# Kernel tuning notes

Measured on AMD Instinct MI355X. Metric: run time of the kernel, lower is better.

Reference implementation:

```python
import jax, jax.numpy as jnp
import numpy as np
from itertools import permutations

BLOCK = 64  # GroupLinear block_size


def _dist_bucket_table():
    # replicates self.distance: log2-style bucketing of token distances [0,1024)
    t = np.zeros(1024, dtype=np.int32)
    for i, th in enumerate([2, 4, 8, 16, 32, 64, 128, 256, 512]):
        t[th:] = i + 1
    return jnp.asarray(t)


def setup_inputs() -> dict:
    key = jax.random.key(0)
    ks = jax.random.split(key, 12)
    B, S, H, NH = 4, 512, 768, 12
    E, TAG, TE, TD, R = 24, 7, 20, 20, 97
    DIN = 2 * H + TE + TD
    hidden_state = jax.random.normal(ks[0], (B, S, H), jnp.float32)
    attention = jax.random.uniform(ks[1], (B, NH, S, S), jnp.float32)
    attention_mask = jnp.ones((B, S), jnp.float32)
    head = jnp.sort(jax.random.randint(ks[2], (B, E), 0, S), axis=-1)
    tail = jnp.sort(jax.random.randint(ks[3], (B, E), 0, S), axis=-1)
    entity_type = jax.random.randint(ks[4], (B, E), 0, TAG)
    type_table = jax.random.normal(ks[5], (TAG, TE), jnp.float32) * 0.02
    dis_table = jax.random.normal(ks[6], (20, TD), jnp.float32) * 0.02
    Wh = jax.random.normal(ks[7], (DIN, H), jnp.float32) * (1.0 / np.sqrt(DIN))
    bh = jnp.zeros((H,), jnp.float32)
    Wt = jax.random.normal(ks[8], (DIN, H), jnp.float32) * (1.0 / np.sqrt(DIN))
    bt = jnp.zeros((H,), jnp.float32)
    # GroupLinear weight reshaped to [n_blocks, BLOCK, BLOCK, R]
    clsW = jax.random.normal(ks[9], (H // BLOCK, BLOCK, BLOCK, R), jnp.float32) * (1.0 / np.sqrt(H * BLOCK))
    clsb = jnp.zeros((R,), jnp.float32)
    return dict(hidden_state=hidden_state, attention=attention,
                attention_mask=attention_mask, head=head, tail=tail,
                entity_type=entity_type, type_table=type_table,
                dis_table=dis_table, Wh=Wh, bh=bh, Wt=Wt, bt=bt,
                clsW=clsW, clsb=clsb)


def reference(hidden_state, attention, attention_mask, head, tail, entity_type,
              type_table, dis_table, Wh, bh, Wt, bt, clsW, clsb):
    E = head.shape[1]
    hts = jnp.asarray(list(permutations(range(E), 2)), dtype=jnp.int32)  # [P,2]
    i0, i1 = hts[:, 0], hts[:, 1]
    dtab = _dist_bucket_table()
    att = attention.sum(axis=1)  # [B,S,S] sum over heads

    def per_sample(h, a, m, hd, tl, et):
        # h:[S,H] a:[S,S] m:[S] hd,tl,et:[E]
        ent_feat = (h[hd] + h[tl]) * 0.5          # [E,H]
        ent_att = (a[hd] + a[tl]) * 0.5           # [E,S]
        ent_tf = type_table[et]                   # [E,TE]
        head_f, tail_f = ent_feat[i0], ent_feat[i1]      # [P,H]
        ht_att = ent_att[i0] * ent_att[i1] * m[None, :]  # [P,S]
        head_ty, tail_ty = ent_tf[i0], ent_tf[i1]        # [P,TE]
        d = dtab[jnp.abs(tl[i0] - hd[i1])]               # [P]
        ht_dist = dis_table[d]                           # [P,TD]
        ht_att = ht_att / (ht_att.sum(-1, keepdims=True) + 1e-20)
        ht_info = ht_att @ h                             # [P,H]
        all_h = jnp.concatenate([head_f, ht_info, head_ty, ht_dist], axis=-1)
        all_t = jnp.concatenate([tail_f, ht_info, tail_ty, ht_dist], axis=-1)
        return all_h, all_t

    all_h, all_t = jax.vmap(per_sample)(hidden_state, att, attention_mask,
                                        head, tail, entity_type)
    all_h = all_h.reshape(-1, all_h.shape[-1])  # [B*P, DIN]
    all_t = all_t.reshape(-1, all_t.shape[-1])
    h1 = jnp.tanh(all_h @ Wh + bh)              # [L,H]
    t1 = jnp.tanh(all_t @ Wt + bt)
    L, H = h1.shape
    nb = H // BLOCK
    x1 = h1.reshape(L, nb, BLOCK)
    x2 = t1.reshape(L, nb, BLOCK)
    # GroupLinear: per-block outer product then linear, fused as einsum
    logits = jnp.einsum('lnb,lnc,nbcr->lr', x1, x2, clsW) + clsb  # [L,R]
    return logits
```

## Files before the change

### kernel.cpp

```cpp
#include <hip/hip_runtime.h>
#include <hip/hip_bf16.h>
#include <math.h>

#define B_ 4
#define S_ 512
#define H_ 768
#define NH_ 12
#define E_ 24
#define TE_ 20
#define TD_ 20
#define R_ 97
#define DIN_ 1576
#define KPAD_ 1600
#define KS_MLP 50
#define MF_MLP 140
#define KS_HTI 16
#define P_ 552
#define L_ 2208
#define NB_ 12
#define NF_ 7

typedef __bf16 bf16x8 __attribute__((ext_vector_type(8)));
typedef float f32x4 __attribute__((ext_vector_type(4)));

__device__ __forceinline__ unsigned short f2bf(float f) {
  union { float f; unsigned u; } c; c.f = f;
  unsigned r = c.u + 0x7FFF + ((c.u >> 16) & 1);
  return (unsigned short)(r >> 16);
}
__device__ __forceinline__ float bf2f(unsigned short b) {
  union { unsigned u; float f; } c; c.u = ((unsigned)b) << 16;
  return c.f;
}
__device__ __forceinline__ unsigned pk2(float a, float b) {
  return (unsigned)f2bf(a) | ((unsigned)f2bf(b) << 16);
}
__device__ __forceinline__ void gload_lds16(const uint4* g, uint4* l) {
  __builtin_amdgcn_global_load_lds(
      (const __attribute__((address_space(1))) unsigned*)(const void*)g,
      (__attribute__((address_space(3))) unsigned*)(void*)l, 16, 0, 0);
}

__global__ void ent_prep(const float* __restrict__ attn, const float* __restrict__ hs,
                         const int* __restrict__ head, const int* __restrict__ tail,
                         float* __restrict__ ent_att, float* __restrict__ ent_feat) {
  int be = blockIdx.x;
  int b = be / E_;
  int hd = head[be], tl = tail[be];
  int tid = threadIdx.x;
  const float* abase = attn + (size_t)b * NH_ * S_ * S_;
  for (int s = tid; s < S_; s += 256) {
    float acc = 0.f;
#pragma unroll
    for (int nh = 0; nh < NH_; ++nh) {
      const float* ap = abase + (size_t)nh * S_ * S_;
      acc += ap[(size_t)hd * S_ + s] + ap[(size_t)tl * S_ + s];
    }
    ent_att[(size_t)be * S_ + s] = 0.5f * acc;
  }
  const float* hb = hs + (size_t)b * S_ * H_;
  for (int k = tid; k < H_; k += 256) {
    ent_feat[(size_t)be * H_ + k] = 0.5f * (hb[(size_t)hd * H_ + k] + hb[(size_t)tl * H_ + k]);
  }
}

__global__ void pair_att(const float* __restrict__ ent_att, const float* __restrict__ mask,
                         const int* __restrict__ head, const int* __restrict__ tail,
                         const int* __restrict__ etype,
                         float* __restrict__ ht_att, int* __restrict__ meta) {
  int l = blockIdx.x;
  int b = l / P_, p = l % P_;
  int i0 = p / (E_ - 1), rem = p % (E_ - 1);
  int i1 = rem + (rem >= i0 ? 1 : 0);
  int tid = threadIdx.x;
  if (tid == 0) {
    meta[0 * L_ + l] = b * E_ + i0;
    meta[1 * L_ + l] = b * E_ + i1;
    meta[2 * L_ + l] = etype[b * E_ + i0];
    meta[3 * L_ + l] = etype[b * E_ + i1];
    int d = abs(tail[b * E_ + i0] - head[b * E_ + i1]);
    int bk = (d >= 2) + (d >= 4) + (d >= 8) + (d >= 16) + (d >= 32) +
             (d >= 64) + (d >= 128) + (d >= 256) + (d >= 512);
    meta[4 * L_ + l] = bk;
  }
  const float* a0 = ent_att + (size_t)(b * E_ + i0) * S_;
  const float* a1 = ent_att + (size_t)(b * E_ + i1) * S_;
  const float* m = mask + (size_t)b * S_;
  float v0 = a0[tid] * a1[tid] * m[tid];
  float v1 = a0[tid + 256] * a1[tid + 256] * m[tid + 256];
  float loc = v0 + v1;
  for (int o = 32; o > 0; o >>= 1) loc += __shfl_down(loc, o, 64);
  __shared__ float red[4];
  if ((tid & 63) == 0) red[tid >> 6] = loc;
  __syncthreads();
  float tot = red[0] + red[1] + red[2] + red[3];
  float inv = 1.f / (tot + 1e-20f);
  ht_att[(size_t)l * S_ + tid] = v0 * inv;
  ht_att[(size_t)l * S_ + tid + 256] = v1 * inv;
}

__global__ void pack_hs(const float* __restrict__ hs, uint4* __restrict__ hsP) {
  int u = blockIdx.x * 256 + threadIdx.x;
  if (u >= B_ * KS_HTI * 48 * 64) return;
  int lane = u & 63;
  int t = u >> 6;
  int nt16 = t % 48;
  int t2 = t / 48;
  int ks = t2 % KS_HTI;
  int b = t2 / KS_HTI;
  int n = nt16 * 16 + (lane & 15);
  int k0 = ks * 32 + ((lane >> 4) << 3);
  const float* src = hs + (size_t)b * S_ * H_;
  unsigned w[4];
#pragma unroll
  for (int q = 0; q < 4; ++q) {
    int k = k0 + 2 * q;
    w[q] = pk2(src[(size_t)k * H_ + n], src[(size_t)(k + 1) * H_ + n]);
  }
  uint4 o; o.x = w[0]; o.y = w[1]; o.z = w[2]; o.w = w[3];
  hsP[u] = o;
}

__global__ void pack_Wmlp(const float* __restrict__ Wh, const float* __restrict__ Wt,
                          uint4* __restrict__ WpH, uint4* __restrict__ WpT) {
  int u = blockIdx.x * 256 + threadIdx.x;
  if (u >= KS_MLP * 48 * 64) return;
  const float* W = blockIdx.y ? Wt : Wh;
  uint4* Wp = blockIdx.y ? WpT : WpH;
  int lane = u & 63;
  int t = u >> 6;
  int nt16 = t % 48;
  int ks = t / 48;
  int n = nt16 * 16 + (lane & 15);
  int k0 = ks * 32 + ((lane >> 4) << 3);
  unsigned w[4];
#pragma unroll
  for (int q = 0; q < 4; ++q) {
    int k = k0 + 2 * q;
    float v0 = (k < DIN_) ? W[(size_t)k * H_ + n] : 0.f;
    float v1 = (k + 1 < DIN_) ? W[(size_t)(k + 1) * H_ + n] : 0.f;
    w[q] = pk2(v0, v1);
  }
  uint4 o; o.x = w[0]; o.y = w[1]; o.z = w[2]; o.w = w[3];
  Wp[u] = o;
}

__global__ void pack_allx(const float* __restrict__ ent_feat, const float* __restrict__ ht_info,
                          const float* __restrict__ ttab, const float* __restrict__ dtab,
                          const int* __restrict__ meta,
                          uint4* __restrict__ axH, uint4* __restrict__ axT) {
  int idx = blockIdx.x * 256 + threadIdx.x;
  int lane = idx & 63;
  int unit = idx >> 6;
  int half = unit / (MF_MLP * KS_MLP);
  int rem = unit % (MF_MLP * KS_MLP);
  int mf = rem / KS_MLP, ks = rem % KS_MLP;
  int row = mf * 16 + (lane & 15);
  int k = ks * 32 + ((lane >> 4) << 3);
  uint4 d; d.x = d.y = d.z = d.w = 0;
  if (row < L_) {
    int frow = meta[half * L_ + row];
    int trow = meta[(2 + half) * L_ + row];
    int db = meta[4 * L_ + row];
    if (k < 768) {
      const float* p = ent_feat + (size_t)frow * H_ + k;
      float4 v0 = *(const float4*)p, v1 = *(const float4*)(p + 4);
      d.x = pk2(v0.x, v0.y); d.y = pk2(v0.z, v0.w);
      d.z = pk2(v1.x, v1.y); d.w = pk2(v1.z, v1.w);
    } else if (k < 1536) {
      const float* p = ht_info + (size_t)row * H_ + (k - 768);
      float4 v0 = *(const float4*)p, v1 = *(const float4*)(p + 4);
      d.x = pk2(v0.x, v0.y); d.y = pk2(v0.z, v0.w);
      d.z = pk2(v1.x, v1.y); d.w = pk2(v1.z, v1.w);
    } else {
      float v[8];
#pragma unroll
      for (int j = 0; j < 8; ++j) {
        int e = k + j;
        v[j] = (e < 1556) ? ttab[trow * TE_ + (e - 1536)]
             : (e < 1576) ? dtab[db * TD_ + (e - 1556)] : 0.f;
      }
      d.x = pk2(v[0], v[1]); d.y = pk2(v[2], v[3]);
      d.z = pk2(v[4], v[5]); d.w = pk2(v[6], v[7]);
    }
  }
  (half ? axT : axH)[(size_t)rem * 64 + lane] = d;
}

__global__ __launch_bounds__(256) void htinfo_mfma(
    const float* __restrict__ htatt, const uint4* __restrict__ hsP,
    float* __restrict__ htinfo) {
  int b = blockIdx.z;
  int m0 = blockIdx.x * 64;
  int nt0 = blockIdx.y * 4;
  int tid = threadIdx.x;
  int wave = tid >> 6, lane = tid & 63;
  int wm = wave & 1, wn = wave >> 1;
  __shared__ __align__(16) uint4 Ash[2][512];
  __shared__ __align__(16) uint4 Bsh[2][512];

  f32x4 acc[2][2];
#pragma unroll
  for (int i = 0; i < 2; ++i)
#pragma unroll
    for (int j = 0; j < 2; ++j) acc[i][j] = (f32x4){0.f, 0.f, 0.f, 0.f};

  auto stageB = [&](int s, int buf) {
#pragma unroll
    for (int i = 0; i < 2; ++i) {
      int c = wave * 2 + i;
      int ntl = c >> 1, kslot = c & 1;
      gload_lds16(hsP + ((size_t)(b * KS_HTI + s * 2 + kslot) * 48 + nt0 + ntl) * 64 + lane,
                  &Bsh[buf][c * 64]);
    }
  };
  auto gatherA = [&](int s, int c, uint4& d) {
    int mfl = c >> 1, kslot = c & 1;
    int row = m0 + mfl * 16 + (lane & 15);
    if (row >= P_) { d.x = d.y = d.z = d.w = 0; return; }
    int k = s * 64 + kslot * 32 + ((lane >> 4) << 3);
    const float* p = htatt + ((size_t)b * P_ + row) * S_ + k;
    float4 v0 = *(const float4*)p, v1 = *(const float4*)(p + 4);
    d.x = pk2(v0.x, v0.y); d.y = pk2(v0.z, v0.w);
    d.z = pk2(v1.x, v1.y); d.w = pk2(v1.z, v1.w);
  };

  {
    uint4 a0_, a1_;
    gatherA(0, wave, a0_); gatherA(0, wave + 4, a1_);
    Ash[0][wave * 64 + lane] = a0_;
    Ash[0][(wave + 4) * 64 + lane] = a1_;
    stageB(0, 0);
  }
  __syncthreads();

  for (int s = 0; s < 8; ++s) {
    int cur = s & 1, nxt = cur ^ 1;
    bool more = (s + 1 < 8);
    uint4 aN0, aN1;
    if (more) {
      stageB(s + 1, nxt);
      gatherA(s + 1, wave, aN0); gatherA(s + 1, wave + 4, aN1);
    }
    bf16x8 af[2][2], bf[2][2];
#pragma unroll
    for (int mf = 0; mf < 2; ++mf)
#pragma unroll
      for (int kc = 0; kc < 2; ++kc)
        af[mf][kc] = *(const bf16x8*)&Ash[cur][((wm * 2 + mf) * 2 + kc) * 64 + lane];
#pragma unroll
    for (int nf = 0; nf < 2; ++nf)
#pragma unroll
      for (int kc = 0; kc < 2; ++kc)
        bf[nf][kc] = *(const bf16x8*)&Bsh[cur][((wn * 2 + nf) * 2 + kc) * 64 + lane];
#pragma unroll
    for (int kc = 0; kc < 2; ++kc)
#pragma unroll
      for (int nf = 0; nf < 2; ++nf)
#pragma unroll
        for (int mf = 0; mf < 2; ++mf)
          acc[mf][nf] = __builtin_amdgcn_mfma_f32_16x16x32_bf16(af[mf][kc], bf[nf][kc], acc[mf][nf], 0, 0, 0);
    if (more) {
      Ash[nxt][wave * 64 + lane] = aN0;
      Ash[nxt][(wave + 4) * 64 + lane] = aN1;
    }
    __syncthreads();
  }

#pragma unroll
  for (int mf = 0; mf < 2; ++mf)
#pragma unroll
    for (int nf = 0; nf < 2; ++nf) {
      int n = nt0 * 16 + (wn * 2 + nf) * 16 + (lane & 15);
#pragma unroll
      for (int reg = 0; reg < 4; ++reg) {
        int l = m0 + (wm * 2 + mf) * 16 + ((lane >> 4) << 2) + reg;
        if (l < P_)
          htinfo[((size_t)b * P_ + l) * H_ + n] = acc[mf][nf][reg];
      }
    }
}

__global__ __launch_bounds__(256) void mlp_mfma(
    const uint4* __restrict__ Apk_h, const uint4* __restrict__ Apk_t,
    const uint4* __restrict__ Wp_h, const uint4* __restrict__ Wp_t,
    const float* __restrict__ bh, const float* __restrict__ bt,
    float* __restrict__ h1, float* __restrict__ t1) {
  int half = blockIdx.z;
  const uint4* Apk = half ? Apk_t : Apk_h;
  const uint4* Wp = half ? Wp_t : Wp_h;
  const float* bias = half ? bt : bh;
  float* out = half ? t1 : h1;
  int mf0 = blockIdx.x * 4;
  int nt0 = blockIdx.y * 4;
  int tid = threadIdx.x;
  int wave = tid >> 6, lane = tid & 63;
  int wm = wave & 1, wn = wave >> 1;
  __shared__ __align__(16) uint4 Ash[2][512];
  __shared__ __align__(16) uint4 Bsh[2][512];

  f32x4 acc[2][2];
#pragma unroll
  for (int i = 0; i < 2; ++i)
#pragma unroll
    for (int j = 0; j < 2; ++j) acc[i][j] = (f32x4){0.f, 0.f, 0.f, 0.f};

  auto stage = [&](int s, int buf) {
#pragma unroll
    for (int i = 0; i < 2; ++i) {
      int c = wave * 2 + i;
      int cl = c >> 1, kslot = c & 1;
      gload_lds16(Apk + ((size_t)(mf0 + cl) * KS_MLP + s * 2 + kslot) * 64 + lane,
                  &Ash[buf][c * 64]);
      gload_lds16(Wp + ((size_t)(s * 2 + kslot) * 48 + nt0 + cl) * 64 + lane,
                  &Bsh[buf][c * 64]);
    }
  };

  stage(0, 0);
  __syncthreads();

  for (int s = 0; s < 25; ++s) {
    int cur = s & 1, nxt = cur ^ 1;
    if (s + 1 < 25) stage(s + 1, nxt);
    bf16x8 af[2][2], bf[2][2];
#pragma unroll
    for (int mf = 0; mf < 2; ++mf)
#pragma unroll
      for (int kc = 0; kc < 2; ++kc)
        af[mf][kc] = *(const bf16x8*)&Ash[cur][((wm * 2 + mf) * 2 + kc) * 64 + lane];
#pragma unroll
    for (int nf = 0; nf < 2; ++nf)
#pragma unroll
      for (int kc = 0; kc < 2; ++kc)
        bf[nf][kc] = *(const bf16x8*)&Bsh[cur][((wn * 2 + nf) * 2 + kc) * 64 + lane];
#pragma unroll
    for (int kc = 0; kc < 2; ++kc)
#pragma unroll
      for (int nf = 0; nf < 2; ++nf)
#pragma unroll
        for (int mf = 0; mf < 2; ++mf)
          acc[mf][nf] = __builtin_amdgcn_mfma_f32_16x16x32_bf16(af[mf][kc], bf[nf][kc], acc[mf][nf], 0, 0, 0);
    __syncthreads();
  }

#pragma unroll
  for (int mf = 0; mf < 2; ++mf)
#pragma unroll
    for (int nf = 0; nf < 2; ++nf) {
      int n = nt0 * 16 + (wn * 2 + nf) * 16 + (lane & 15);
      float bv = bias[n];
#pragma unroll
      for (int reg = 0; reg < 4; ++reg) {
        int l = (mf0 + wm * 2 + mf) * 16 + ((lane >> 4) << 2) + reg;
        if (l < L_)
          out[(size_t)l * H_ + n] = tanhf(acc[mf][nf][reg] + bv);
      }
    }
}

__global__ void pack_w(const float* __restrict__ clsW, uint4* __restrict__ Wfrag) {
  int nb = blockIdx.x;
  __shared__ float Wls[64][98];
  int tid = threadIdx.x;
  const float* src = clsW + (size_t)nb * 64 * R_;
  for (int idx = tid; idx < 64 * R_; idx += 256) {
    Wls[idx / R_][idx % R_] = src[idx];
  }
  __syncthreads();
  for (int u = tid; u < 896; u += 256) {
    int nf = u >> 7;
    int kc = (u >> 6) & 1;
    int lane = u & 63;
    int r = (lane & 15) + 16 * nf;
    unsigned w[4];
#pragma unroll
    for (int q = 0; q < 4; ++q) {
      int c0 = ((lane >> 4) << 3) + 2 * q + 32 * kc;
      float v0 = (r < R_) ? Wls[c0][r] : 0.f;
      float v1 = (r < R_) ? Wls[c0 + 1][r] : 0.f;
      w[q] = (unsigned)f2bf(v0) | ((unsigned)f2bf(v1) << 16);
    }
    uint4 o; o.x = w[0]; o.y = w[1]; o.z = w[2]; o.w = w[3];
    Wfrag[(size_t)nb * 896 + u] = o;
  }
}

__global__ __launch_bounds__(256) void bilinear_mfma(
    const float* __restrict__ h1, const float* __restrict__ t1,
    const uint4* __restrict__ Wfrag, float* __restrict__ part,
    float* __restrict__ part2) {
  int blk = blockIdx.x;
  int xcd = blk & 7;
  int slot = blk >> 3;
  int pg = slot / 36;
  int j = slot % 36;
  int p = pg * 8 + xcd;
  int n = p >> 1, z = p & 1;
  int l0 = j * 64;
  int tid = threadIdx.x;
  int wave = tid >> 6, lane = tid & 63;
  int wm = wave & 1, kh = wave >> 1;
  __shared__ __align__(16) uint4 Wl[2][2][7][64];
  __shared__ unsigned short x1s[32][66];

  for (int i = tid; i < 512; i += 256) {
    int row = i >> 3, cq = (i & 7) * 4;
    float4 v = make_float4(0, 0, 0, 0);
    if (l0 + row < L_)
      v = *(const float4*)(h1 + (size_t)(l0 + row) * H_ + n * 64 + z * 32 + cq);
    x1s[cq + 0][row] = f2bf(v.x);
    x1s[cq + 1][row] = f2bf(v.y);
    x1s[cq + 2][row] = f2bf(v.z);
    x1s[cq + 3][row] = f2bf(v.w);
  }

  float x2f[2][2][8];
#pragma unroll
  for (int mf = 0; mf < 2; ++mf) {
    int row = l0 + wm * 32 + mf * 16 + (lane & 15);
#pragma unroll
    for (int kc = 0; kc < 2; ++kc) {
      float4 v0 = make_float4(0, 0, 0, 0), v1 = v0;
      if (row < L_) {
        const float* ptr = t1 + (size_t)row * H_ + n * 64 + kc * 32 + ((lane >> 4) << 3);
        v0 = *(const float4*)ptr;
        v1 = *(const float4*)(ptr + 4);
      }
      x2f[mf][kc][0] = v0.x; x2f[mf][kc][1] = v0.y;
      x2f[mf][kc][2] = v0.z; x2f[mf][kc][3] = v0.w;
      x2f[mf][kc][4] = v1.x; x2f[mf][kc][5] = v1.y;
      x2f[mf][kc][6] = v1.z; x2f[mf][kc][7] = v1.w;
    }
  }

  f32x4 acc[2][NF_];
#pragma unroll
  for (int mf = 0; mf < 2; ++mf)
#pragma unroll
    for (int nf = 0; nf < NF_; ++nf)
      acc[mf][nf] = (f32x4){0.f, 0.f, 0.f, 0.f};

  const uint4* gbase = Wfrag + (size_t)n * 64 * 896;
  auto stage = [&](int s, int buf) {
    int b = z * 32 + kh * 16 + (s >> 1);
    int kc = s & 1;
    const uint4* gs = gbase + (size_t)b * 896 + kc * 64 + lane;
    if (wm == 0) {
#pragma unroll
      for (int nf = 0; nf < 4; ++nf)
        gload_lds16(gs + nf * 128, &Wl[kh][buf][nf][0]);
    } else {
#pragma unroll
      for (int nf = 4; nf < 7; ++nf)
        gload_lds16(gs + nf * 128, &Wl[kh][buf][nf][0]);
    }
  };

  stage(0, 0);
  __syncthreads();

  for (int s = 0; s < 32; ++s) {
    int cur = s & 1, nxt = cur ^ 1;
    if (s + 1 < 32) stage(s + 1, nxt);
    int bl = kh * 16 + (s >> 1);
    int kc = s & 1;
    bf16x8 afr[2];
#pragma unroll
    for (int mf = 0; mf < 2; ++mf) {
      float x1v = bf2f(x1s[bl][wm * 32 + mf * 16 + (lane & 15)]);
#pragma unroll
      for (int jj = 0; jj < 8; ++jj)
        afr[mf][jj] = (__bf16)(x1v * x2f[mf][kc][jj]);
    }
#pragma unroll
    for (int nf = 0; nf < NF_; ++nf) {
      bf16x8 bfr = *(const bf16x8*)&Wl[kh][cur][nf][lane];
#pragma unroll
      for (int mf = 0; mf < 2; ++mf)
        acc[mf][nf] = __builtin_amdgcn_mfma_f32_16x16x32_bf16(
            afr[mf], bfr, acc[mf][nf], 0, 0, 0);
    }
    __syncthreads();
  }

  float* red = (float*)&Wl[0][0][0][0];
  int rbase = (wm * 64 + lane) * 56;
  if (kh == 1) {
#pragma unroll
    for (int mf = 0; mf < 2; ++mf)
#pragma unroll
      for (int nf = 0; nf < NF_; ++nf)
        *(f32x4*)&red[rbase + (mf * NF_ + nf) * 4] = acc[mf][nf];
  }
  __syncthreads();
  if (kh == 0) {
    float* dst = (z == 0) ? part : part2;
#pragma unroll
    for (int mf = 0; mf < 2; ++mf) {
#pragma unroll
      for (int nf = 0; nf < NF_; ++nf) {
        acc[mf][nf] += *(const f32x4*)&red[rbase + (mf * NF_ + nf) * 4];
        int r = nf * 16 + (lane & 15);
        if (r < R_) {
#pragma unroll
          for (int reg = 0; reg < 4; ++reg) {
            int l = l0 + wm * 32 + mf * 16 + ((lane >> 4) << 2) + reg;
            if (l < L_)
              dst[((size_t)n * L_ + l) * R_ + r] = acc[mf][nf][reg];
          }
        }
      }
    }
  }
}

__global__ void reduce_logits(const float* __restrict__ part, const float* __restrict__ part2,
                              const float* __restrict__ clsb, float* __restrict__ out) {
  int idx = blockIdx.x * 256 + threadIdx.x;
  if (idx < L_ * R_) {
    int r = idx % R_;
    float s = clsb[r];
#pragma unroll
    for (int nn = 0; nn < NB_; ++nn)
      s += part[(size_t)nn * L_ * R_ + idx] + part2[(size_t)nn * L_ * R_ + idx];
    out[idx] = s;
  }
}

extern "C" void kernel_launch(void* const* d_in, const int* in_sizes, int n_in,
                              void* d_out, int out_size, void* d_ws, size_t ws_size,
                              hipStream_t stream) {
  const float* hs   = (const float*)d_in[0];
  const float* attn = (const float*)d_in[1];
  const float* mask = (const float*)d_in[2];
  const int*   head = (const int*)d_in[3];
  const int*   tail = (const int*)d_in[4];
  const int*   etyp = (const int*)d_in[5];
  const float* ttab = (const float*)d_in[6];
  const float* dtab = (const float*)d_in[7];
  const float* Wh   = (const float*)d_in[8];
  const float* bh   = (const float*)d_in[9];
  const float* Wt   = (const float*)d_in[10];
  const float* bt   = (const float*)d_in[11];
  const float* clsW = (const float*)d_in[12];
  const float* clsb = (const float*)d_in[13];
  float* out = (float*)d_out;

  float* ws = (float*)d_ws;
  float* ent_att  = ws; ws += (size_t)B_ * E_ * S_;
  float* ent_feat = ws; ws += (size_t)B_ * E_ * H_;
  float* ht_att   = ws; ws += (size_t)L_ * S_;
  float* ht_info  = ws; ws += (size_t)L_ * H_;
  float* h1       = ws; ws += (size_t)L_ * H_;
  float* t1       = ws; ws += (size_t)L_ * H_;
  float* part     = ws; ws += (size_t)NB_ * L_ * R_;
  uint4* Wpack_h  = (uint4*)ws; ws += (size_t)KS_MLP * 48 * 64 * 4;
  uint4* Wpack_t  = (uint4*)ws; ws += (size_t)KS_MLP * 48 * 64 * 4;
  uint4* hsPack   = (uint4*)ws; ws += (size_t)B_ * KS_HTI * 48 * 64 * 4;
  uint4* Wfrag    = (uint4*)ws; ws += (size_t)NB_ * 64 * 896 * 4;
  uint4* allx_h   = (uint4*)ws; ws += (size_t)MF_MLP * KS_MLP * 64 * 4;
  uint4* allx_t   = (uint4*)ws; ws += (size_t)MF_MLP * KS_MLP * 64 * 4;
  int* meta = (int*)ws;
  float* part2 = (float*)allx_h;

  ent_prep<<<B_ * E_, 256, 0, stream>>>(attn, hs, head, tail, ent_att, ent_feat);
  pair_att<<<L_, 256, 0, stream>>>(ent_att, mask, head, tail, etyp, ht_att, meta);
  pack_hs<<<(B_ * KS_HTI * 48 * 64) / 256, 256, 0, stream>>>(hs, hsPack);
  htinfo_mfma<<<dim3(9, 12, B_), 256, 0, stream>>>(ht_att, hsPack, ht_info);
  pack_Wmlp<<<dim3((KS_MLP * 48 * 64) / 256, 2), 256, 0, stream>>>(Wh, Wt, Wpack_h, Wpack_t);
  pack_allx<<<(2 * MF_MLP * KS_MLP * 64) / 256, 256, 0, stream>>>(
      ent_feat, ht_info, ttab, dtab, meta, allx_h, allx_t);
  mlp_mfma<<<dim3(35, 12, 2), 256, 0, stream>>>(allx_h, allx_t,
      Wpack_h, Wpack_t, bh, bt, h1, t1);
  pack_w<<<NB_ * 64, 256, 0, stream>>>(clsW, Wfrag);
  bilinear_mfma<<<864, 256, 0, stream>>>(h1, t1, Wfrag, part, part2);
  reduce_logits<<<(L_ * R_ + 255) / 256, 256, 0, stream>>>(part, part2, clsb, out);
}
```

Measured before the change: 127.5 us.

## Load bilinear weight fragments directly into registers instead of staging through LDS

```diff
diff --git a/kernel.cpp b/kernel.cpp
--- a/kernel.cpp
+++ b/kernel.cpp
@@ -401,8 +401,8 @@
   int tid = threadIdx.x;
   int wave = tid >> 6, lane = tid & 63;
   int wm = wave & 1, kh = wave >> 1;
-  __shared__ __align__(16) uint4 Wl[2][2][7][64];
   __shared__ unsigned short x1s[32][66];
+  __shared__ float red[128 * 56];
 
   for (int i = tid; i < 512; i += 256) {
     int row = i >> 3, cq = (i & 7) * 4;
@@ -441,28 +441,27 @@
     for (int nf = 0; nf < NF_; ++nf)
       acc[mf][nf] = (f32x4){0.f, 0.f, 0.f, 0.f};
 
+  __syncthreads();
+
   const uint4* gbase = Wfrag + (size_t)n * 64 * 896;
-  auto stage = [&](int s, int buf) {
-    int b = z * 32 + kh * 16 + (s >> 1);
-    int kc = s & 1;
-    const uint4* gs = gbase + (size_t)b * 896 + kc * 64 + lane;
-    if (wm == 0) {
-#pragma unroll
-      for (int nf = 0; nf < 4; ++nf)
-        gload_lds16(gs + nf * 128, &Wl[kh][buf][nf][0]);
-    } else {
-#pragma unroll
-      for (int nf = 4; nf < 7; ++nf)
-        gload_lds16(gs + nf * 128, &Wl[kh][buf][nf][0]);
-    }
-  };
-
-  stage(0, 0);
-  __syncthreads();
-
+  int bbase = z * 32 + kh * 16;
+  uint4 wreg[7];
+  {
+    const uint4* gs = gbase + (size_t)bbase * 896 + lane;
+#pragma unroll
+    for (int nf = 0; nf < 7; ++nf) wreg[nf] = gs[nf * 128];
+  }
+
+#pragma unroll 2
   for (int s = 0; s < 32; ++s) {
-    int cur = s & 1, nxt = cur ^ 1;
-    if (s + 1 < 32) stage(s + 1, nxt);
+    uint4 wnx[7];
+    if (s + 1 < 32) {
+      int b = bbase + ((s + 1) >> 1);
+      int kcn = (s + 1) & 1;
+      const uint4* gs = gbase + (size_t)b * 896 + kcn * 64 + lane;
+#pragma unroll
+      for (int nf = 0; nf < 7; ++nf) wnx[nf] = gs[nf * 128];
+    }
     int bl = kh * 16 + (s >> 1);
     int kc = s & 1;
     bf16x8 afr[2];
@@ -475,16 +474,17 @@
     }
 #pragma unroll
     for (int nf = 0; nf < NF_; ++nf) {
-      bf16x8 bfr = *(const bf16x8*)&Wl[kh][cur][nf][lane];
+      union { uint4 u; bf16x8 b; } cvt;
+      cvt.u = wreg[nf];
 #pragma unroll
       for (int mf = 0; mf < 2; ++mf)
         acc[mf][nf] = __builtin_amdgcn_mfma_f32_16x16x32_bf16(
-            afr[mf], bfr, acc[mf][nf], 0, 0, 0);
-    }
-    __syncthreads();
-  }
-
-  float* red = (float*)&Wl[0][0][0][0];
+            afr[mf], cvt.b, acc[mf][nf], 0, 0, 0);
+    }
+#pragma unroll
+    for (int nf = 0; nf < 7; ++nf) wreg[nf] = wnx[nf];
+  }
+
   int rbase = (wm * 64 + lane) * 56;
   if (kh == 1) {
 #pragma unroll
```

Result: no change. 126.3 us (-0.9%).
